# Performance work log

Hardware: AMD Instinct MI355X
Metric: run time of the kernel (lower is better)

The kernel has to match this reference:

```python
import jax, jax.numpy as jnp
import numpy as np

N_NODES = 50000
N_EDGES = 800000
IN_DIM = 256
OUT_DIM = 64


def setup_inputs() -> dict:
    key = jax.random.key(0)
    k1, k2, k3, k4 = jax.random.split(key, 4)
    feat = jax.random.normal(k1, (N_NODES, IN_DIM), dtype=jnp.float32)
    W1 = jax.random.normal(k2, (IN_DIM, OUT_DIM), dtype=jnp.float32) / np.sqrt(IN_DIM)
    b1 = jnp.zeros((OUT_DIM,), dtype=jnp.float32)
    W2 = jax.random.normal(k3, (OUT_DIM, OUT_DIM), dtype=jnp.float32) / np.sqrt(OUT_DIM)
    b2 = jnp.zeros((OUT_DIM,), dtype=jnp.float32)
    edge_index = jax.random.randint(k4, (2, N_EDGES), 0, N_NODES, dtype=jnp.int64)
    return {"feat": feat, "W1": W1, "b1": b1, "W2": W2, "b2": b2,
            "edge_index": edge_index}


def _gcn_norm(edge_index, num_nodes):
    # PyG GCNConv default: add self-loops, symmetric normalization.
    loops = jnp.arange(num_nodes, dtype=edge_index.dtype)
    src = jnp.concatenate([edge_index[0], loops])  # [E+N]
    dst = jnp.concatenate([edge_index[1], loops])  # [E+N]
    deg = jax.ops.segment_sum(jnp.ones_like(dst, dtype=jnp.float32), dst,
                              num_segments=num_nodes)
    dinv = jnp.where(deg > 0, jax.lax.rsqrt(deg), 0.0)
    norm = dinv[src] * dinv[dst]  # [E+N]
    return src, dst, norm


def _gcn_conv(x, W, b, src, dst, norm, num_nodes):
    h = x @ W                                   # [N, out]
    msg = h[src] * norm[:, None]                # gather + scale, [E+N, out]
    agg = jax.ops.segment_sum(msg, dst, num_segments=num_nodes)
    return agg + b


def reference(feat, W1, b1, W2, b2, edge_index):
    n = feat.shape[0]
    src, dst, norm = _gcn_norm(edge_index, n)
    # Layer 1: GCNConv -> ReLU (dropout is identity in eval mode)
    z = jax.nn.relu(_gcn_conv(feat, W1, b1, src, dst, norm, n))
    # Layer 2
    z = jax.nn.relu(_gcn_conv(z, W2, b2, src, dst, norm, n))
    return z
```

## Files before the change

kernel.cpp:

```cpp
#include <hip/hip_runtime.h>
#include <hip/hip_bf16.h>

#define N_NODES 50000
#define N_EDGES 800000
#define IN_DIM  256
#define OUT_DIM 64
#define CHUNKE  4096
#define NCHK    196
#define NBKT    196
#define STAGE   12288

using bf16x8 = __attribute__((ext_vector_type(8))) __bf16;
using f32x4  = __attribute__((ext_vector_type(4))) float;
using u32x4  = __attribute__((ext_vector_type(4))) unsigned int;

union BFu { u32x4 u; bf16x8 b; };

__device__ __forceinline__ void split_pack(float x0, float x1,
                                           unsigned& hi, unsigned& lo) {
    unsigned u0 = __float_as_uint(x0), u1 = __float_as_uint(x1);
    hi = (u1 & 0xFFFF0000u) | (u0 >> 16);
    float h0 = __uint_as_float(u0 & 0xFFFF0000u);
    float h1 = __uint_as_float(u1 & 0xFFFF0000u);
    unsigned r0 = __float_as_uint(x0 - h0);
    unsigned r1 = __float_as_uint(x1 - h1);
    lo = (r1 & 0xFFFF0000u) | (r0 >> 16);
}

__device__ __forceinline__ unsigned short bf16_rn(float x) {
    unsigned u = __float_as_uint(x);
    unsigned r = u + 0x7FFFu + ((u >> 16) & 1u);
    return (unsigned short)(r >> 16);
}

template <int K>
__device__ __forceinline__ void gemm_body(int gbid, const float* __restrict__ X,
                                          const float* __restrict__ W,
                                          unsigned short* __restrict__ H,
                                          char* lds) {
    constexpr int NS = K / 32;
    const int lane = threadIdx.x & 63;
    const int wave = threadIdx.x >> 6;
    const int lm   = lane & 15;
    const int kg   = lane >> 4;

    BFu bhi[NS], blo[NS];
#pragma unroll
    for (int s = 0; s < NS; ++s) {
#pragma unroll
        for (int jp = 0; jp < 4; ++jp) {
            float w0 = W[(size_t)(s * 32 + kg * 8 + 2 * jp)     * 64 + wave * 16 + lm];
            float w1 = W[(size_t)(s * 32 + kg * 8 + 2 * jp + 1) * 64 + wave * 16 + lm];
            unsigned h, l;
            split_pack(w0, w1, h, l);
            bhi[s].u[jp] = h;
            blo[s].u[jp] = l;
        }
    }

    const int srow = threadIdx.x >> 2;
    const int skc  = (threadIdx.x & 3) * 8;
    int gr = gbid * 64 + srow;
    const float* xs = X + (size_t)((gr < N_NODES) ? gr : (N_NODES - 1)) * K;

    f32x4 acc[4] = {};

    float4 c0 = *(const float4*)(xs + skc);
    float4 c1 = *(const float4*)(xs + skc + 4);

#pragma unroll
    for (int s = 0; s < NS; ++s) {
        unsigned short* a_hi = (unsigned short*)(lds + (s & 1) * 8192);
        unsigned short* a_lo = a_hi + 64 * 32;

        BFu h_, l_;
        unsigned h, l;
        split_pack(c0.x, c0.y, h, l); h_.u[0] = h; l_.u[0] = l;
        split_pack(c0.z, c0.w, h, l); h_.u[1] = h; l_.u[1] = l;
        split_pack(c1.x, c1.y, h, l); h_.u[2] = h; l_.u[2] = l;
        split_pack(c1.z, c1.w, h, l); h_.u[3] = h; l_.u[3] = l;
        *(u32x4*)(a_hi + srow * 32 + skc) = h_.u;
        *(u32x4*)(a_lo + srow * 32 + skc) = l_.u;

        if (s + 1 < NS) {
            c0 = *(const float4*)(xs + (s + 1) * 32 + skc);
            c1 = *(const float4*)(xs + (s + 1) * 32 + skc + 4);
        }

        __syncthreads();

#pragma unroll
        for (int m = 0; m < 4; ++m) {
            BFu ah, al;
            ah.u = *(const u32x4*)(a_hi + (m * 16 + lm) * 32 + kg * 8);
            al.u = *(const u32x4*)(a_lo + (m * 16 + lm) * 32 + kg * 8);
            acc[m] = __builtin_amdgcn_mfma_f32_16x16x32_bf16(ah.b, bhi[s].b, acc[m], 0, 0, 0);
            acc[m] = __builtin_amdgcn_mfma_f32_16x16x32_bf16(ah.b, blo[s].b, acc[m], 0, 0, 0);
            acc[m] = __builtin_amdgcn_mfma_f32_16x16x32_bf16(al.b, bhi[s].b, acc[m], 0, 0, 0);
        }
    }

    const int c = wave * 16 + lm;
#pragma unroll
    for (int m = 0; m < 4; ++m) {
#pragma unroll
        for (int t = 0; t < 4; ++t) {
            int r = gbid * 64 + m * 16 + kg * 4 + t;
            if (r < N_NODES) H[(size_t)r * 64 + c] = bf16_rn(acc[m][t]);
        }
    }
}

template <int K>
__global__ __launch_bounds__(256) void fused_hist_gemm1(const void* __restrict__ edges,
                                                        int* __restrict__ src32,
                                                        int* __restrict__ dst32,
                                                        int* __restrict__ hist,
                                                        const float* __restrict__ X,
                                                        const float* __restrict__ W,
                                                        unsigned short* __restrict__ H) {
    __shared__ char lds[16384];
    if ((int)blockIdx.x < NCHK) {
        int* h  = (int*)lds;
        int* nz = (int*)(lds + 1024);
        if (threadIdx.x == 0) *nz = 0;
        h[threadIdx.x] = 0;
        __syncthreads();
        if (((const unsigned int*)edges)[2 * threadIdx.x + 1] != 0u) *nz = 1;
        __syncthreads();
        const int is64 = (*nz == 0);
        const int base = blockIdx.x * CHUNKE;
        for (int i = threadIdx.x; i < CHUNKE; i += 256) {
            int e = base + i;
            if (e < N_EDGES) {
                int s, d;
                if (is64) {
                    s = (int)((const long long*)edges)[e];
                    d = (int)((const long long*)edges)[(long long)N_EDGES + e];
                } else {
                    s = ((const int*)edges)[e];
                    d = ((const int*)edges)[(long long)N_EDGES + e];
                }
                src32[e] = s;
                dst32[e] = d;
                atomicAdd(&h[d >> 8], 1);
            }
        }
        __syncthreads();
        hist[blockIdx.x * 256 + threadIdx.x] = h[threadIdx.x];
    } else {
        gemm_body<K>((int)blockIdx.x - NCHK, X, W, H, lds);
    }
}

__global__ __launch_bounds__(64) void radix_scan(int* __restrict__ hist,
                                                 int* __restrict__ bsum) {
    const int b = blockIdx.x, l = threadIdx.x;
    int carry = 0;
#pragma unroll
    for (int seg = 0; seg < 4; ++seg) {
        int c = seg * 64 + l;
        int v = (c < NCHK) ? hist[c * 256 + b] : 0;
        int incl = v;
        for (int s = 1; s < 64; s <<= 1) {
            int t = __shfl_up(incl, s);
            if (l >= s) incl += t;
        }
        if (c < NCHK) hist[c * 256 + b] = incl - v + carry;
        carry += __shfl(incl, 63);
    }
    if (l == 0) bsum[b] = carry;
}

__global__ __launch_bounds__(256) void radix_scatter(const int* __restrict__ src32,
                                                     const int* __restrict__ dst32,
                                                     const int* __restrict__ hist,
                                                     const int* __restrict__ bsum,
                                                     int2* __restrict__ ebuf) {
    __shared__ int lcur[256];
    __shared__ int sm[256];
    __shared__ int sbase[256];
    const int t = threadIdx.x;
    int v = bsum[t];
    sm[t] = v;
    lcur[t] = 0;
    __syncthreads();
    for (int s = 1; s < 256; s <<= 1) {
        int tv = 0;
        if (t >= s) tv = sm[t - s];
        __syncthreads();
        if (t >= s) sm[t] += tv;
        __syncthreads();
    }
    sbase[t] = sm[t] - v;
    __syncthreads();
    const int base = blockIdx.x * CHUNKE;
    for (int i = t; i < CHUNKE; i += 256) {
        int e = base + i;
        if (e < N_EDGES) {
            int s = src32[e], d = dst32[e];
            int bin = d >> 8;
            int loc = atomicAdd(&lcur[bin], 1);
            int pos = sbase[bin] + hist[blockIdx.x * 256 + bin] + loc;
            ebuf[pos] = make_int2(s, d);
        }
    }
}

__global__ __launch_bounds__(256) void bucket_finalize(const int2* __restrict__ ebuf,
                                                       const int* __restrict__ bsum,
                                                       float* __restrict__ dinv,
                                                       int* __restrict__ off,
                                                       int* __restrict__ csr_src) {
    __shared__ int hist[256];
    __shared__ int sm[256];
    __shared__ int cur[256];
    __shared__ int stage[STAGE];
    __shared__ int beg_s, end_s;
    const int b = blockIdx.x, t = threadIdx.x;

    int v = bsum[t];
    sm[t] = v;
    __syncthreads();
    for (int s = 1; s < 256; s <<= 1) {
        int tv = 0;
        if (t >= s) tv = sm[t - s];
        __syncthreads();
        if (t >= s) sm[t] += tv;
        __syncthreads();
    }
    if (t == b) { beg_s = sm[t] - v; end_s = sm[t]; }
    __syncthreads();
    const int beg = beg_s, end = end_s, size = end - beg;

    hist[t] = 0;
    __syncthreads();
    for (int e = beg + t; e < end; e += 256) atomicAdd(&hist[ebuf[e].y & 255], 1);
    __syncthreads();

    v = hist[t];
    sm[t] = v;
    __syncthreads();
    for (int s = 1; s < 256; s <<= 1) {
        int tv = 0;
        if (t >= s) tv = sm[t - s];
        __syncthreads();
        if (t >= s) sm[t] += tv;
        __syncthreads();
    }
    int pre = sm[t] - v;

    int node = b * 256 + t;
    if (node < N_NODES) {
        off[node] = beg + pre;
        dinv[node] = rsqrtf((float)(v + 1));
    }
    if (b == NBKT - 1 && t == 0) off[N_NODES] = end;

    cur[t] = pre;
    __syncthreads();

    if (size <= STAGE) {
        for (int e = beg + t; e < end; e += 256) {
            int2 ed = ebuf[e];
            int p = atomicAdd(&cur[ed.y & 255], 1);
            stage[p] = ed.x;
        }
        __syncthreads();
        for (int i = t; i < size; i += 256) csr_src[beg + i] = stage[i];
    } else {
        for (int e = beg + t; e < end; e += 256) {
            int2 ed = ebuf[e];
            int p = atomicAdd(&cur[ed.y & 255], 1);
            csr_src[beg + p] = ed.x;
        }
    }
}

template <int K>
__global__ __launch_bounds__(256) void gemm_mfma(const float* __restrict__ X,
                                                 const float* __restrict__ W,
                                                 unsigned short* __restrict__ H) {
    __shared__ char lds[16384];
    gemm_body<K>((int)blockIdx.x, X, W, H, lds);
}

__device__ __forceinline__ float bf2f(unsigned short u) {
    return __uint_as_float((unsigned)u << 16);
}

__global__ __launch_bounds__(256) void agg_csr(const unsigned short* __restrict__ H,
                                               const float* __restrict__ dinv,
                                               const float* __restrict__ b,
                                               const int* __restrict__ off,
                                               const int* __restrict__ csr_src,
                                               float* __restrict__ out) {
    int wid  = (blockIdx.x * 256 + threadIdx.x) >> 6;
    int lane = threadIdx.x & 63;
    if (wid >= N_NODES) return;
    float dd = dinv[wid];
    float acc = bf2f(H[(size_t)wid * 64 + lane]) * dd;
    int beg = off[wid], end = off[wid + 1];
    for (int k0 = beg; k0 < end; k0 += 64) {
        int myk = k0 + lane;
        int   s_l  = (myk < end) ? csr_src[myk] : 0;
        float ds_l = (myk < end) ? dinv[s_l] : 0.f;
        int cnt = min(64, end - k0);
        int i = 0;
        for (; i + 8 <= cnt; i += 8) {
            float v[8], nm[8];
#pragma unroll
            for (int jj = 0; jj < 8; ++jj) {
                int s  = __shfl(s_l, i + jj);
                nm[jj] = __shfl(ds_l, i + jj);
                v[jj]  = bf2f(H[(size_t)s * 64 + lane]);
            }
#pragma unroll
            for (int jj = 0; jj < 8; ++jj) acc = fmaf(v[jj], nm[jj], acc);
        }
        for (; i < cnt; ++i) {
            int   s  = __shfl(s_l, i);
            float nm = __shfl(ds_l, i);
            acc = fmaf(bf2f(H[(size_t)s * 64 + lane]), nm, acc);
        }
    }
    out[(size_t)wid * 64 + lane] = fmaxf(fmaf(acc, dd, b[lane]), 0.f);
}

extern "C" void kernel_launch(void* const* d_in, const int* in_sizes, int n_in,
                              void* d_out, int out_size, void* d_ws, size_t ws_size,
                              hipStream_t stream) {
    const float* feat = (const float*)d_in[0];
    const float* W1   = (const float*)d_in[1];
    const float* b1   = (const float*)d_in[2];
    const float* W2   = (const float*)d_in[3];
    const float* b2   = (const float*)d_in[4];
    const void*  edges = d_in[5];
    float* out = (float*)d_out;

    char* ws = (char*)d_ws;
    const size_t SZ_E = (size_t)N_EDGES * 4;
    int*   bsum    = (int*)(ws + 2048);
    int*   hist    = (int*)(ws + 4096);
    float* dinv    = (float*)(ws + 4096 + 204800);
    int*   off     = (int*)(ws + 4096 + 204800 + 204800);
    size_t o = 4096 + 3 * 204800;
    int*   src32   = (int*)(ws + o);              o += SZ_E;
    int*   dst32   = (int*)(ws + o);              o += SZ_E;
    int2*  ebuf    = (int2*)(ws + o);             o += 2 * SZ_E;
    int*   csr_src = (int*)(ws + o);              o += SZ_E;
    unsigned short* H = (unsigned short*)(ws + o);

    const int NB_G = (N_NODES + 63) / 64;
    const int NB_W = (N_NODES * 64 + 255) / 256;

    fused_hist_gemm1<IN_DIM><<<NCHK + NB_G, 256, 0, stream>>>(
        edges, src32, dst32, hist, feat, W1, H);
    radix_scan<<<256, 64, 0, stream>>>(hist, bsum);
    radix_scatter<<<NCHK, 256, 0, stream>>>(src32, dst32, hist, bsum, ebuf);
    bucket_finalize<<<NBKT, 256, 0, stream>>>(ebuf, bsum, dinv, off, csr_src);

    agg_csr<<<NB_W, 256, 0, stream>>>(H, dinv, b1, off, csr_src, out);

    gemm_mfma<OUT_DIM><<<NB_G, 256, 0, stream>>>(out, W2, H);
    agg_csr<<<NB_W, 256, 0, stream>>>(H, dinv, b2, off, csr_src, out);
}
```

Before: 114.8 us.

## Pack edges into 32-bit words and fuse layer-1 aggregation with layer-2 GEMM

Edges are packed into a single 32-bit word (bucket, 16-bit source, low destination byte), which halves the intermediate edge traffic through the radix-sort stages. The layer-1 aggregation kernel now also computes the 64x64 layer-2 projection per node, using wave shuffles against W2 held in LDS, and writes bf16 H2 directly. This removes one kernel launch and the fp32 round trip of the intermediate activations. The 16-bit source field only fits node ids below 65536, and the second GEMM moves from MFMA to scalar FMA in full fp32.

```diff
diff --git a/kernel.cpp b/kernel.cpp
--- a/kernel.cpp
+++ b/kernel.cpp
@@ -13,6 +13,11 @@
 using bf16x8 = __attribute__((ext_vector_type(8))) __bf16;
 using f32x4  = __attribute__((ext_vector_type(4))) float;
 using u32x4  = __attribute__((ext_vector_type(4))) unsigned int;
+
+#define EPACK(s, d)   ((unsigned)((d) >> 8) << 24 | (unsigned)(s) << 8 | ((d) & 255))
+#define E_BIN(p)      ((p) >> 24)
+#define E_SRC(p)      (((p) >> 8) & 0xFFFFu)
+#define E_DLOW(p)     ((p) & 255u)
 
 union BFu { u32x4 u; bf16x8 b; };
 
@@ -31,6 +36,10 @@
     unsigned u = __float_as_uint(x);
     unsigned r = u + 0x7FFFu + ((u >> 16) & 1u);
     return (unsigned short)(r >> 16);
+}
+
+__device__ __forceinline__ float bf2f(unsigned short u) {
+    return __uint_as_float((unsigned)u << 16);
 }
 
 template <int K>
@@ -113,8 +122,7 @@
 
 template <int K>
 __global__ __launch_bounds__(256) void fused_hist_gemm1(const void* __restrict__ edges,
-                                                        int* __restrict__ src32,
-                                                        int* __restrict__ dst32,
+                                                        unsigned* __restrict__ epack,
                                                         int* __restrict__ hist,
                                                         const float* __restrict__ X,
                                                         const float* __restrict__ W,
@@ -141,8 +149,7 @@
                     s = ((const int*)edges)[e];
                     d = ((const int*)edges)[(long long)N_EDGES + e];
                 }
-                src32[e] = s;
-                dst32[e] = d;
+                epack[e] = EPACK(s, d);
                 atomicAdd(&h[d >> 8], 1);
             }
         }
@@ -172,11 +179,10 @@
     if (l == 0) bsum[b] = carry;
 }
 
-__global__ __launch_bounds__(256) void radix_scatter(const int* __restrict__ src32,
-                                                     const int* __restrict__ dst32,
+__global__ __launch_bounds__(256) void radix_scatter(const unsigned* __restrict__ epack,
                                                      const int* __restrict__ hist,
                                                      const int* __restrict__ bsum,
-                                                     int2* __restrict__ ebuf) {
+                                                     unsigned* __restrict__ ebuf) {
     __shared__ int lcur[256];
     __shared__ int sm[256];
     __shared__ int sbase[256];
@@ -198,16 +204,16 @@
     for (int i = t; i < CHUNKE; i += 256) {
         int e = base + i;
         if (e < N_EDGES) {
-            int s = src32[e], d = dst32[e];
-            int bin = d >> 8;
+            unsigned p = epack[e];
+            int bin = (int)E_BIN(p);
             int loc = atomicAdd(&lcur[bin], 1);
             int pos = sbase[bin] + hist[blockIdx.x * 256 + bin] + loc;
-            ebuf[pos] = make_int2(s, d);
-        }
-    }
-}
-
-__global__ __launch_bounds__(256) void bucket_finalize(const int2* __restrict__ ebuf,
+            ebuf[pos] = p;
+        }
+    }
+}
+
+__global__ __launch_bounds__(256) void bucket_finalize(const unsigned* __restrict__ ebuf,
                                                        const int* __restrict__ bsum,
                                                        float* __restrict__ dinv,
                                                        int* __restrict__ off,
@@ -235,7 +241,8 @@
 
     hist[t] = 0;
     __syncthreads();
-    for (int e = beg + t; e < end; e += 256) atomicAdd(&hist[ebuf[e].y & 255], 1);
+    for (int e = beg + t; e < end; e += 256)
+        atomicAdd(&hist[E_DLOW(ebuf[e])], 1);
     __syncthreads();
 
     v = hist[t];
@@ -262,31 +269,70 @@
 
     if (size <= STAGE) {
         for (int e = beg + t; e < end; e += 256) {
-            int2 ed = ebuf[e];
-            int p = atomicAdd(&cur[ed.y & 255], 1);
-            stage[p] = ed.x;
+            unsigned p = ebuf[e];
+            int q = atomicAdd(&cur[E_DLOW(p)], 1);
+            stage[q] = (int)E_SRC(p);
         }
         __syncthreads();
         for (int i = t; i < size; i += 256) csr_src[beg + i] = stage[i];
     } else {
         for (int e = beg + t; e < end; e += 256) {
-            int2 ed = ebuf[e];
-            int p = atomicAdd(&cur[ed.y & 255], 1);
-            csr_src[beg + p] = ed.x;
-        }
-    }
-}
-
-template <int K>
-__global__ __launch_bounds__(256) void gemm_mfma(const float* __restrict__ X,
-                                                 const float* __restrict__ W,
-                                                 unsigned short* __restrict__ H) {
-    __shared__ char lds[16384];
-    gemm_body<K>((int)blockIdx.x, X, W, H, lds);
-}
-
-__device__ __forceinline__ float bf2f(unsigned short u) {
-    return __uint_as_float((unsigned)u << 16);
+            unsigned p = ebuf[e];
+            int q = atomicAdd(&cur[E_DLOW(p)], 1);
+            csr_src[beg + q] = (int)E_SRC(p);
+        }
+    }
+}
+
+__global__ __launch_bounds__(256) void agg1_gemm2(const unsigned short* __restrict__ H,
+                                                  const float* __restrict__ dinv,
+                                                  const float* __restrict__ b1v,
+                                                  const int* __restrict__ off,
+                                                  const int* __restrict__ csr_src,
+                                                  const float* __restrict__ W2,
+                                                  unsigned short* __restrict__ H2) {
+    __shared__ float w2s[64 * 64];
+    for (int i = threadIdx.x; i < 64 * 16; i += 256)
+        ((float4*)w2s)[i] = ((const float4*)W2)[i];
+    __syncthreads();
+
+    int wid  = (blockIdx.x * 256 + threadIdx.x) >> 6;
+    int lane = threadIdx.x & 63;
+    float dd = dinv[wid];
+    float acc = bf2f(H[(size_t)wid * 64 + lane]) * dd;
+    int beg = off[wid], end = off[wid + 1];
+    for (int k0 = beg; k0 < end; k0 += 64) {
+        int myk = k0 + lane;
+        int   s_l  = (myk < end) ? csr_src[myk] : 0;
+        float ds_l = (myk < end) ? dinv[s_l] : 0.f;
+        int cnt = min(64, end - k0);
+        int i = 0;
+        for (; i + 8 <= cnt; i += 8) {
+            float v[8], nm[8];
+#pragma unroll
+            for (int jj = 0; jj < 8; ++jj) {
+                int s  = __shfl(s_l, i + jj);
+                nm[jj] = __shfl(ds_l, i + jj);
+                v[jj]  = bf2f(H[(size_t)s * 64 + lane]);
+            }
+#pragma unroll
+            for (int jj = 0; jj < 8; ++jj) acc = fmaf(v[jj], nm[jj], acc);
+        }
+        for (; i < cnt; ++i) {
+            int   s  = __shfl(s_l, i);
+            float nm = __shfl(ds_l, i);
+            acc = fmaf(bf2f(H[(size_t)s * 64 + lane]), nm, acc);
+        }
+    }
+    float zv = fmaxf(fmaf(acc, dd, b1v[lane]), 0.f);
+
+    float acc2 = 0.f;
+#pragma unroll 8
+    for (int k = 0; k < 64; ++k) {
+        float bz = __shfl(zv, k);
+        acc2 = fmaf(bz, w2s[k * 64 + lane], acc2);
+    }
+    H2[(size_t)wid * 64 + lane] = bf16_rn(acc2);
 }
 
 __global__ __launch_bounds__(256) void agg_csr(const unsigned short* __restrict__ H,
@@ -340,28 +386,27 @@
 
     char* ws = (char*)d_ws;
     const size_t SZ_E = (size_t)N_EDGES * 4;
-    int*   bsum    = (int*)(ws + 2048);
-    int*   hist    = (int*)(ws + 4096);
-    float* dinv    = (float*)(ws + 4096 + 204800);
-    int*   off     = (int*)(ws + 4096 + 204800 + 204800);
+    int*      bsum    = (int*)(ws + 2048);
+    int*      hist    = (int*)(ws + 4096);
+    float*    dinv    = (float*)(ws + 4096 + 204800);
+    int*      off     = (int*)(ws + 4096 + 2 * 204800);
     size_t o = 4096 + 3 * 204800;
-    int*   src32   = (int*)(ws + o);              o += SZ_E;
-    int*   dst32   = (int*)(ws + o);              o += SZ_E;
-    int2*  ebuf    = (int2*)(ws + o);             o += 2 * SZ_E;
-    int*   csr_src = (int*)(ws + o);              o += SZ_E;
-    unsigned short* H = (unsigned short*)(ws + o);
+    unsigned* epack   = (unsigned*)(ws + o);      o += SZ_E;
+    unsigned* ebuf    = (unsigned*)(ws + o);      o += SZ_E;
+    int*      csr_src = (int*)(ws + o);           o += SZ_E;
+    unsigned short* H  = (unsigned short*)(ws + o); o += (size_t)N_NODES * 64 * 2;
+    unsigned short* H2 = (unsigned short*)(ws + o);
 
     const int NB_G = (N_NODES + 63) / 64;
     const int NB_W = (N_NODES * 64 + 255) / 256;
 
     fused_hist_gemm1<IN_DIM><<<NCHK + NB_G, 256, 0, stream>>>(
-        edges, src32, dst32, hist, feat, W1, H);
+        edges, epack, hist, feat, W1, H);
     radix_scan<<<256, 64, 0, stream>>>(hist, bsum);
-    radix_scatter<<<NCHK, 256, 0, stream>>>(src32, dst32, hist, bsum, ebuf);
+    radix_scatter<<<NCHK, 256, 0, stream>>>(epack, hist, bsum, ebuf);
     bucket_finalize<<<NBKT, 256, 0, stream>>>(ebuf, bsum, dinv, off, csr_src);
 
-    agg_csr<<<NB_W, 256, 0, stream>>>(H, dinv, b1, off, csr_src, out);
-
-    gemm_mfma<OUT_DIM><<<NB_G, 256, 0, stream>>>(out, W2, H);
-    agg_csr<<<NB_W, 256, 0, stream>>>(H, dinv, b2, off, csr_src, out);
-}
+    agg1_gemm2<<<NB_W, 256, 0, stream>>>(H, dinv, b1, off, csr_src, W2, H2);
+
+    agg_csr<<<NB_W, 256, 0, stream>>>(H2, dinv, b2, off, csr_src, out);
+}
```

Result: slower. 142.3 us (+24.0%).
